# Kernel tuning notes

Measured on AMD Instinct MI355X. Metric: run time of the kernel, lower is better.

## Reference

```python
import jax, jax.numpy as jnp
import numpy as np
import math

D = 1024
FFN = 4096
NHEADS = 8
HEAD_DIM = D // NHEADS
RL_DIM = 4
LN_EPS = 1e-5


def _layer_norm(x, gamma, beta):
    mu = jnp.mean(x, axis=-1, keepdims=True)
    var = jnp.var(x, axis=-1, keepdims=True)
    return (x - mu) * jax.lax.rsqrt(var + LN_EPS) * gamma + beta


def setup_inputs() -> dict:
    key = jax.random.key(0)
    ks = jax.random.split(key, 12)
    B, L = 2, 2048
    s = 1.0 / math.sqrt(D)
    inp = {
        "h": jax.random.normal(ks[0], (B, L, D), dtype=jnp.float32),
        "rh": jax.random.normal(ks[1], (B, L, RL_DIM), dtype=jnp.float32),
        "Wq": jax.random.normal(ks[2], (D, D), dtype=jnp.float32) * s,
        "Wk": jax.random.normal(ks[3], (D, D), dtype=jnp.float32) * s,
        "Wv": jax.random.normal(ks[4], (D, D), dtype=jnp.float32) * s,
        "Wo": jax.random.normal(ks[5], (D, D), dtype=jnp.float32) * s,
        "Wrk": jax.random.normal(ks[6], (RL_DIM, RL_DIM), dtype=jnp.float32) * 0.5,
        "Wrq": jax.random.normal(ks[7], (RL_DIM, RL_DIM), dtype=jnp.float32) * 0.5,
        "W1": jax.random.normal(ks[8], (D, FFN), dtype=jnp.float32) * s,
        "b1": jnp.zeros((FFN,), dtype=jnp.float32),
        "W2": jax.random.normal(ks[9], (FFN, D), dtype=jnp.float32) / math.sqrt(FFN),
        "b2": jnp.zeros((D,), dtype=jnp.float32),
        "g1": jnp.ones((D,), dtype=jnp.float32),
        "be1": jnp.zeros((D,), dtype=jnp.float32),
        "g2": jnp.ones((D,), dtype=jnp.float32),
        "be2": jnp.zeros((D,), dtype=jnp.float32),
    }
    return inp


def reference(h, rh, Wq, Wk, Wv, Wo, Wrk, Wrq, W1, b1, W2, b2, g1, be1, g2, be2):
    B, L, _ = h.shape
    q = h @ Wq  # [B, L, D]
    k = h @ Wk
    v = h @ Wv
    # Faithful to the torch code: .view() reshapes (NOT transposes).
    q_ = q.reshape(B, NHEADS, L, HEAD_DIM)
    k_ = k.reshape(B, NHEADS, L, HEAD_DIM)
    v_ = v.reshape(B, NHEADS, L, HEAD_DIM)
    k_t = k_.reshape(B, NHEADS, HEAD_DIM, L)  # reshape, not transpose, as in source
    score = jnp.einsum("bnld,bndm->bnlm", q_, k_t) / math.sqrt(HEAD_DIM)
    # relative-position bias (rl=True path)
    r_k = rh @ Wrk  # [B, L, rl_dim]
    r_q = rh @ Wrq
    r_q_ = r_q[:, None]  # [B, 1, L, rl_dim]
    r_k_t = r_k[:, None].reshape(B, 1, RL_DIM, L)  # reshape, as in source
    score = score + jnp.einsum("bnlr,bnrm->bnlm", r_q_, r_k_t) / 2.0
    attn = jax.nn.softmax(score, axis=-1)
    context = jnp.einsum("bnlm,bnmd->bnld", attn, v_)
    h_sa = context.reshape(B, L, D) @ Wo
    h1 = _layer_norm(h_sa + h, g1, be1)
    hf = jax.nn.relu(h1 @ W1 + b1) @ W2 + b2
    h2 = _layer_norm(h1 + hf, g2, be2)
    return h2
```

## Files before the change

### kernel.cpp

```cpp
#include <hip/hip_runtime.h>

typedef __bf16 bf16;
typedef __bf16 bf16x8 __attribute__((ext_vector_type(8)));
typedef __bf16 bf16x4 __attribute__((ext_vector_type(4)));
typedef float  f32x4  __attribute__((ext_vector_type(4)));

#define D_     1024
#define FFN_   4096
#define NH_    8
#define HD_    128
#define L_     2048
#define B_     2
#define ROWS_  4096
#define PAIRS_ 16
#define KT_    64
#define PSTR   72
#define ALPHA_  0.08838834764831845f
#define RSCALE_ 5.656854249492381f

__device__ __forceinline__ void async16(const bf16* g, bf16* l) {
    __builtin_amdgcn_global_load_lds(
        (const __attribute__((address_space(1))) unsigned int*)g,
        (__attribute__((address_space(3))) unsigned int*)l, 16, 0, 0);
}
__device__ __forceinline__ f32x4 MFMA(bf16x8 a, bf16x8 b, f32x4 c) {
    return __builtin_amdgcn_mfma_f32_16x16x32_bf16(a, b, c, 0, 0, 0);
}

__global__ void cvt_bf16_kernel(const float* __restrict__ in, bf16* __restrict__ out) {
    long i = ((long)blockIdx.x * 256 + threadIdx.x) * 4;
    float4 v = *(const float4*)(in + i);
    bf16x4 o = {(bf16)v.x, (bf16)v.y, (bf16)v.z, (bf16)v.w};
    *(bf16x4*)(out + i) = o;
}

template<typename TI>
__global__ void transpose_to_bf16(const TI* __restrict__ in, bf16* __restrict__ out,
                                  int r, int c, long sIn, long sOut) {
    __shared__ bf16 t[32][33];
    long zi = (long)blockIdx.z * sIn;
    long zo = (long)blockIdx.z * sOut;
    int x0 = blockIdx.x * 32, y0 = blockIdx.y * 32;
    int tx = threadIdx.x & 31, ty = threadIdx.x >> 5;
#pragma unroll
    for (int i = 0; i < 4; i++)
        t[ty + i * 8][tx] = (bf16)in[zi + (long)(y0 + ty + i * 8) * c + x0 + tx];
    __syncthreads();
#pragma unroll
    for (int i = 0; i < 4; i++)
        out[zo + (long)(x0 + ty + i * 8) * r + y0 + tx] = t[tx][ty + i * 8];
}

__global__ void rqk_kernel(const float* __restrict__ rh, const float* __restrict__ Wrq,
                           const float* __restrict__ Wrk, float* __restrict__ rq,
                           float* __restrict__ rk) {
    int t = blockIdx.x * 256 + threadIdx.x;
    float4 r = *(const float4*)(rh + (long)t * 4);
    float q[4], k[4];
#pragma unroll
    for (int c = 0; c < 4; c++) {
        q[c] = r.x * Wrq[c] + r.y * Wrq[4 + c] + r.z * Wrq[8 + c] + r.w * Wrq[12 + c];
        k[c] = r.x * Wrk[c] + r.y * Wrk[4 + c] + r.z * Wrk[8 + c] + r.w * Wrk[12 + c];
    }
    float4 qo = {q[0], q[1], q[2], q[3]};
    float4 ko = {k[0], k[1], k[2], k[3]};
    *(float4*)(rq + (long)t * 4) = qo;
    *(float4*)(rk + (long)t * 4) = ko;
}

template<int BM, int EPI>
__launch_bounds__(256)
__global__ void gemm128(const bf16* __restrict__ A, const bf16* __restrict__ Bt,
                        void* __restrict__ Cv, const float* __restrict__ bias,
                        int M, int N, int K, int lda, int ldb,
                        long sA, long sB, long sC, float alpha) {
    constexpr int RF = (BM == 128) ? 4 : 2;
    __shared__ __align__(16) bf16 As[BM * 32];
    __shared__ __align__(16) bf16 Bs[128 * 32];
    const int tid  = threadIdx.x;
    const int wave = tid >> 6, lane = tid & 63;
    const int quad = lane >> 4, mr = lane & 15;
    const int bM = blockIdx.x * BM, bN = blockIdx.y * 128;
    A  += (long)blockIdx.z * sA;
    Bt += (long)blockIdx.z * sB;
    const int wr = (wave >> 1) * (BM / 2), wc = (wave & 1) * 64;

    f32x4 acc[RF][4];
#pragma unroll
    for (int r = 0; r < RF; r++)
#pragma unroll
        for (int c = 0; c < 4; c++) { f32x4 z = {0.f, 0.f, 0.f, 0.f}; acc[r][c] = z; }

    const int scol = (lane & 3) * 8;
    const bf16* Ag0; const bf16* Ag1 = nullptr;
    if (BM == 128) {
        const int srow = wave * 32 + (lane >> 2);
        Ag0 = A + (long)(bM + srow) * lda + scol;
        Ag1 = Ag0 + (long)16 * lda;
    } else {
        const int srow = wave * 16 + (lane >> 2);
        Ag0 = A + (long)(bM + srow) * lda + scol;
    }
    const int srowB = wave * 32 + (lane >> 2);
    const bf16* Bg0 = Bt + (long)(bN + srowB) * ldb + scol;
    const bf16* Bg1 = Bg0 + (long)16 * ldb;
    bf16* AsW = As + wave * (BM == 128 ? 1024 : 512);
    bf16* BsW = Bs + wave * 1024;

    for (int k0 = 0; k0 < K; k0 += 32) {
        if (BM == 128) { async16(Ag0, AsW); async16(Ag1, AsW + 512); Ag0 += 32; Ag1 += 32; }
        else           { async16(Ag0, AsW); Ag0 += 32; }
        async16(Bg0, BsW); async16(Bg1, BsW + 512);
        Bg0 += 32; Bg1 += 32;
        __syncthreads();
        bf16x8 af[RF], bfv[4];
#pragma unroll
        for (int r = 0; r < RF; r++)
            af[r] = *(const bf16x8*)(&As[(wr + r * 16 + mr) * 32 + quad * 8]);
#pragma unroll
        for (int c = 0; c < 4; c++)
            bfv[c] = *(const bf16x8*)(&Bs[(wc + c * 16 + mr) * 32 + quad * 8]);
#pragma unroll
        for (int r = 0; r < RF; r++)
#pragma unroll
            for (int c = 0; c < 4; c++)
                acc[r][c] = MFMA(af[r], bfv[c], acc[r][c]);
        __syncthreads();
    }

    const long zC = (long)blockIdx.z * sC;
    float bias_c[4];
    if (EPI & 1) {
#pragma unroll
        for (int c = 0; c < 4; c++) bias_c[c] = bias[bN + wc + c * 16 + mr];
    }
#pragma unroll
    for (int r = 0; r < RF; r++) {
#pragma unroll
        for (int c = 0; c < 4; c++) {
            const long col = bN + wc + c * 16 + mr;
#pragma unroll
            for (int i = 0; i < 4; i++) {
                const long row = bM + wr + r * 16 + quad * 4 + i;
                float v = acc[r][c][i] * alpha;
                if (EPI & 1) v += bias_c[c];
                if (EPI & 2) v = fmaxf(v, 0.f);
                if (EPI & 4) ((bf16*)Cv)[zC + row * (long)N + col] = (bf16)v;
                else         ((float*)Cv)[zC + row * (long)N + col] = v;
            }
        }
    }
}

template<int EPI>
__launch_bounds__(512, 2)
__global__ void gemm256(const bf16* __restrict__ A, const bf16* __restrict__ Bt,
                        void* __restrict__ Cv, const float* __restrict__ bias,
                        int M, int N, int K, int lda, int ldb,
                        long sA, long sB, long sC, float alpha) {
    __shared__ __align__(16) bf16 LA[4][256 * 32];
    __shared__ __align__(16) bf16 LB[4][256 * 32];
    const int tid = threadIdx.x, wave = tid >> 6, lane = tid & 63;
    const int quad = lane >> 4, mr = lane & 15;
    const int wr = wave >> 2, wc = wave & 3;
    const int bM = blockIdx.x * 256, bN = blockIdx.y * 256;
    (void)M;
    A  += (long)blockIdx.z * sA;
    Bt += (long)blockIdx.z * sB;

    const int srow = tid >> 2;
    const int sg   = (((tid & 3) ^ ((tid >> 3) & 3))) * 8;
    const bf16* Ag = A  + (long)(bM + srow) * lda + sg;
    const bf16* Bg = Bt + (long)(bN + srow) * ldb + sg;

    auto stageA = [&](int slot, int kt) {
        const bf16* s = Ag + kt * 32;
        async16(s,                   &LA[slot][wave * 512]);
        async16(s + (long)128 * lda, &LA[slot][4096 + wave * 512]);
    };
    auto stageB = [&](int slot, int kt) {
        const bf16* s = Bg + kt * 32;
        async16(s,                   &LB[slot][wave * 512]);
        async16(s + (long)128 * ldb, &LB[slot][4096 + wave * 512]);
    };

    f32x4 acc[8][4];
#pragma unroll
    for (int f = 0; f < 8; f++)
#pragma unroll
        for (int n = 0; n < 4; n++) { f32x4 z = {0.f, 0.f, 0.f, 0.f}; acc[f][n] = z; }

    const int gsw = (quad ^ ((mr >> 1) & 3)) * 8;

    stageA(0, 0); stageB(0, 0);
    stageA(1, 1); stageB(1, 1);
    stageA(2, 2); stageB(2, 2);
    asm volatile("s_waitcnt vmcnt(8)" ::: "memory");
    __builtin_amdgcn_s_barrier();

    const int NT = K >> 5;
    for (int t = 0; t < NT; ++t) {
        const int slot = t & 3;
        const bf16* As = &LA[slot][0];
        const bf16* Bs = &LB[slot][0];

        bf16x8 a0[4], bb[4];
#pragma unroll
        for (int f = 0; f < 4; f++)
            a0[f] = *(const bf16x8*)(As + (wr * 128 + f * 16 + mr) * 32 + gsw);
#pragma unroll
        for (int n = 0; n < 4; n++)
            bb[n] = *(const bf16x8*)(Bs + (wc * 64 + n * 16 + mr) * 32 + gsw);
        if (t + 3 < NT) stageA((t + 3) & 3, t + 3);
        __builtin_amdgcn_s_barrier();
        asm volatile("s_waitcnt lgkmcnt(0)" ::: "memory");
        __builtin_amdgcn_sched_barrier(0);
        __builtin_amdgcn_s_setprio(1);
#pragma unroll
        for (int f = 0; f < 4; f++)
#pragma unroll
            for (int n = 0; n < 4; n++)
                acc[f][n] = MFMA(a0[f], bb[n], acc[f][n]);
        __builtin_amdgcn_s_setprio(0);
        __builtin_amdgcn_s_barrier();

        bf16x8 a1[4];
#pragma unroll
        for (int f = 0; f < 4; f++)
            a1[f] = *(const bf16x8*)(As + (wr * 128 + 64 + f * 16 + mr) * 32 + gsw);
        if (t + 3 < NT) stageB((t + 3) & 3, t + 3);
        __builtin_amdgcn_s_barrier();
        asm volatile("s_waitcnt lgkmcnt(0)" ::: "memory");
        __builtin_amdgcn_sched_barrier(0);
        __builtin_amdgcn_s_setprio(1);
#pragma unroll
        for (int f = 0; f < 4; f++)
#pragma unroll
            for (int n = 0; n < 4; n++)
                acc[4 + f][n] = MFMA(a1[f], bb[n], acc[4 + f][n]);
        __builtin_amdgcn_s_setprio(0);
        if (t < NT - 3)       asm volatile("s_waitcnt vmcnt(8)" ::: "memory");
        else if (t == NT - 3) asm volatile("s_waitcnt vmcnt(4)" ::: "memory");
        else if (t == NT - 2) asm volatile("s_waitcnt vmcnt(0)" ::: "memory");
        __builtin_amdgcn_s_barrier();
    }

    const long zC = (long)blockIdx.z * sC;
    float bias_c[4];
    if (EPI & 1) {
#pragma unroll
        for (int n = 0; n < 4; n++) bias_c[n] = bias[bN + wc * 64 + n * 16 + mr];
    }
#pragma unroll
    for (int f = 0; f < 8; f++) {
#pragma unroll
        for (int n = 0; n < 4; n++) {
            const long col = bN + wc * 64 + n * 16 + mr;
#pragma unroll
            for (int i = 0; i < 4; i++) {
                const long row = bM + wr * 128 + f * 16 + quad * 4 + i;
                float v = acc[f][n][i] * alpha;
                if (EPI & 1) v += bias_c[n];
                if (EPI & 2) v = fmaxf(v, 0.f);
                if (EPI & 4) ((bf16*)Cv)[zC + row * (long)N + col] = (bf16)v;
                else         ((float*)Cv)[zC + row * (long)N + col] = v;
            }
        }
    }
}

template<int SPLIT>
__launch_bounds__(256, 1)
__global__ void flash_attn(const bf16* __restrict__ qb, const bf16* __restrict__ kT,
                           const bf16* __restrict__ vT, const float* __restrict__ rq,
                           const float* __restrict__ rk, bf16* __restrict__ ctx,
                           float* __restrict__ opart, float* __restrict__ osum) {
    __shared__ __align__(16) bf16  Ksh[KT_ * HD_];
    __shared__ __align__(16) bf16  Vsh[HD_ * KT_];
    __shared__ __align__(16) float rks[4 * KT_];
    __shared__ __align__(16) bf16  Ps[4][32 * PSTR];

    const int tid = threadIdx.x, wave = tid >> 6, lane = tid & 63;
    const int quad = lane >> 4, mr = lane & 15;
    const int pair = blockIdx.y, b = pair >> 3;
    const int ksp = blockIdx.z;
    const int bQ = blockIdx.x * 128;
    const long PB = (long)pair * L_ * HD_;
    const bf16* Qg = qb + PB;
    const bf16* Kg = kT + PB;
    const bf16* Vg = vT + PB;
    const float* rkb = rk + (long)b * L_ * 4;

    bf16x8 Qf[2][4], Qe[2];
#pragma unroll
    for (int f = 0; f < 2; f++) {
#pragma unroll
        for (int t = 0; t < 4; t++)
            Qf[f][t] = *(const bf16x8*)(Qg + (long)(bQ + wave * 32 + f * 16 + mr) * HD_ + t * 32 + quad * 8);
        bf16x8 z = {};
        if (quad == 0) {
            float4 v = *(const float4*)(rq + ((long)b * L_ + bQ + wave * 32 + f * 16 + mr) * 4);
            z[0] = (bf16)(v.x * RSCALE_); z[1] = (bf16)(v.y * RSCALE_);
            z[2] = (bf16)(v.z * RSCALE_); z[3] = (bf16)(v.w * RSCALE_);
        }
        Qe[f] = z;
    }

    bf16x8 ones;
#pragma unroll
    for (int j = 0; j < 8; j++) ones[j] = (bf16)1.0f;

    f32x4 O[2][8], Os[2];
#pragma unroll
    for (int f = 0; f < 2; f++) {
#pragma unroll
        for (int c = 0; c < 8; c++) { f32x4 z = {0.f, 0.f, 0.f, 0.f}; O[f][c] = z; }
        f32x4 z = {0.f, 0.f, 0.f, 0.f}; Os[f] = z;
    }

    const int tile0 = ksp * ((L_ / KT_) / SPLIT);
    const int tile1 = tile0 + (L_ / KT_) / SPLIT;
    for (int kt = tile0; kt < tile1; kt++) {
        const int kt0 = kt * KT_;
#pragma unroll
        for (int it = 0; it < 4; it++) {
            int G = it * 256 + tid;
            int r1 = G >> 4, g1 = (G & 15) ^ (r1 & 15);
            async16(Kg + (long)(kt0 + r1) * HD_ + g1 * 8, &Ksh[(it * 256 + wave * 64) * 8]);
            int r2 = G >> 3, g2 = (G & 7) ^ (r2 & 7);
            async16(Vg + (long)r2 * L_ + kt0 + g2 * 8, &Vsh[(it * 256 + wave * 64) * 8]);
        }
        if (tid < 64) {
            int r3 = tid >> 4, g3 = tid & 15;
            async16((const bf16*)(rkb + (long)r3 * L_ + kt0 + g3 * 4), (bf16*)&rks[0]);
        }
        __syncthreads();

        bf16* PsW = Ps[wave];

        f32x4 sc[4][2];
#pragma unroll
        for (int c = 0; c < 4; c++) {
            f32x4 s0 = {0.f, 0.f, 0.f, 0.f}, s1 = s0;
#pragma unroll
            for (int t = 0; t < 4; t++) {
                bf16x8 kf = *(const bf16x8*)(Ksh + (c * 16 + mr) * HD_ + (((t * 4 + quad) ^ mr) * 8));
                s0 = MFMA(Qf[0][t], kf, s0);
                s1 = MFMA(Qf[1][t], kf, s1);
            }
            bf16x8 ke = {};
            if (quad == 0) {
                ke[0] = (bf16)rks[0 * KT_ + c * 16 + mr];
                ke[1] = (bf16)rks[1 * KT_ + c * 16 + mr];
                ke[2] = (bf16)rks[2 * KT_ + c * 16 + mr];
                ke[3] = (bf16)rks[3 * KT_ + c * 16 + mr];
            }
            s0 = MFMA(Qe[0], ke, s0);
            s1 = MFMA(Qe[1], ke, s1);
            sc[c][0] = s0; sc[c][1] = s1;
        }

#pragma unroll
        for (int f = 0; f < 2; f++) {
#pragma unroll
            for (int i = 0; i < 4; i++) {
                const int prow = (f * 16 + quad * 4 + i) * PSTR;
                PsW[prow + 0 * 16 + mr] = (bf16)__expf(sc[0][f][i] * ALPHA_);
                PsW[prow + 1 * 16 + mr] = (bf16)__expf(sc[1][f][i] * ALPHA_);
                PsW[prow + 2 * 16 + mr] = (bf16)__expf(sc[2][f][i] * ALPHA_);
                PsW[prow + 3 * 16 + mr] = (bf16)__expf(sc[3][f][i] * ALPHA_);
            }
        }

#pragma unroll
        for (int t = 0; t < 2; t++) {
            bf16x8 pf0 = *(const bf16x8*)(PsW + (0 * 16 + mr) * PSTR + t * 32 + quad * 8);
            bf16x8 pf1 = *(const bf16x8*)(PsW + (1 * 16 + mr) * PSTR + t * 32 + quad * 8);
            Os[0] = MFMA(pf0, ones, Os[0]);
            Os[1] = MFMA(pf1, ones, Os[1]);
#pragma unroll
            for (int c2 = 0; c2 < 8; c2++) {
                bf16x8 vf = *(const bf16x8*)(Vsh + (c2 * 16 + mr) * KT_ + (((t * 4 + quad) ^ (mr & 7)) * 8));
                O[0][c2] = MFMA(pf0, vf, O[0][c2]);
                O[1][c2] = MFMA(pf1, vf, O[1][c2]);
            }
        }
        __syncthreads();
    }

    if (SPLIT == 1) {
        bf16* Cg = ctx + PB;
#pragma unroll
        for (int f = 0; f < 2; f++)
#pragma unroll
            for (int i = 0; i < 4; i++) {
                const float inv = 1.f / Os[f][i];
                const long row = bQ + wave * 32 + f * 16 + quad * 4 + i;
#pragma unroll
                for (int c2 = 0; c2 < 8; c2++)
                    Cg[row * HD_ + c2 * 16 + mr] = (bf16)(O[f][c2][i] * inv);
            }
    } else {
        float* Og = opart + (long)ksp * ((long)PAIRS_ * L_ * HD_) + PB;
        float* Sg = osum + (long)ksp * (PAIRS_ * L_) + pair * L_;
#pragma unroll
        for (int f = 0; f < 2; f++)
#pragma unroll
            for (int i = 0; i < 4; i++) {
                const long row = bQ + wave * 32 + f * 16 + quad * 4 + i;
#pragma unroll
                for (int c2 = 0; c2 < 8; c2++)
                    Og[row * HD_ + c2 * 16 + mr] = O[f][c2][i];
                if (mr == 0) Sg[row] = Os[f][i];
            }
    }
}

__global__ void flash_reduce(const float* __restrict__ op, const float* __restrict__ os,
                             bf16* __restrict__ ctx) {
    const long PLHD = (long)PAIRS_ * L_ * HD_;
    long e = ((long)blockIdx.x * 256 + threadIdx.x) * 4;
    long row = e >> 7;
    float4 a = *(const float4*)(op + e);
    float4 b = *(const float4*)(op + PLHD + e);
    float inv = 1.f / (os[row] + os[(long)PAIRS_ * L_ + row]);
    bf16x4 o = {(bf16)((a.x + b.x) * inv), (bf16)((a.y + b.y) * inv),
                (bf16)((a.z + b.z) * inv), (bf16)((a.w + b.w) * inv)};
    *(bf16x4*)(ctx + e) = o;
}

__global__ void layernorm_res(const float* __restrict__ x1, const float* __restrict__ x2,
                              const float* __restrict__ g, const float* __restrict__ be,
                              float* __restrict__ outf, bf16* __restrict__ outb) {
    const int row = blockIdx.x, tid = threadIdx.x;
    const long base = (long)row * D_ + tid * 4;
    float4 a = *(const float4*)(x1 + base);
    float4 b = *(const float4*)(x2 + base);
    float x[4] = {a.x + b.x, a.y + b.y, a.z + b.z, a.w + b.w};
    float s = x[0] + x[1] + x[2] + x[3];
    float s2 = x[0] * x[0] + x[1] * x[1] + x[2] * x[2] + x[3] * x[3];
#pragma unroll
    for (int off = 32; off; off >>= 1) { s += __shfl_xor(s, off, 64); s2 += __shfl_xor(s2, off, 64); }
    __shared__ float ps[4], ps2[4];
    int wave = tid >> 6, lane = tid & 63;
    if (lane == 0) { ps[wave] = s; ps2[wave] = s2; }
    __syncthreads();
    s  = ps[0] + ps[1] + ps[2] + ps[3];
    s2 = ps2[0] + ps2[1] + ps2[2] + ps2[3];
    float mean = s * (1.f / D_);
    float var  = s2 * (1.f / D_) - mean * mean;
    float rstd = rsqrtf(var + 1e-5f);
    float4 gg = *(const float4*)(g + tid * 4);
    float4 bb = *(const float4*)(be + tid * 4);
    float y0 = (x[0] - mean) * rstd * gg.x + bb.x;
    float y1 = (x[1] - mean) * rstd * gg.y + bb.y;
    float y2 = (x[2] - mean) * rstd * gg.z + bb.z;
    float y3 = (x[3] - mean) * rstd * gg.w + bb.w;
    float4 yo = {y0, y1, y2, y3};
    *(float4*)(outf + base) = yo;
    bf16x4 ob = {(bf16)y0, (bf16)y1, (bf16)y2, (bf16)y3};
    *(bf16x4*)(outb + base) = ob;
}

template<int SK>
__global__ void layernorm_res2(const float* __restrict__ parts, const float* __restrict__ b2,
                               const float* __restrict__ x2, const float* __restrict__ g,
                               const float* __restrict__ be, float* __restrict__ outf) {
    const int row = blockIdx.x, tid = threadIdx.x;
    const long base = (long)row * D_ + tid * 4;
    float4 a = *(const float4*)(parts + base);
#pragma unroll
    for (int z = 1; z < SK; z++) {
        float4 p = *(const float4*)(parts + (long)z * ROWS_ * D_ + base);
        a.x += p.x; a.y += p.y; a.z += p.z; a.w += p.w;
    }
    float4 bb2 = *(const float4*)(b2 + tid * 4);
    float4 b = *(const float4*)(x2 + base);
    float x[4] = {a.x + bb2.x + b.x, a.y + bb2.y + b.y, a.z + bb2.z + b.z, a.w + bb2.w + b.w};
    float s = x[0] + x[1] + x[2] + x[3];
    float s2 = x[0] * x[0] + x[1] * x[1] + x[2] * x[2] + x[3] * x[3];
#pragma unroll
    for (int off = 32; off; off >>= 1) { s += __shfl_xor(s, off, 64); s2 += __shfl_xor(s2, off, 64); }
    __shared__ float ps[4], ps2[4];
    int wave = tid >> 6, lane = tid & 63;
    if (lane == 0) { ps[wave] = s; ps2[wave] = s2; }
    __syncthreads();
    s  = ps[0] + ps[1] + ps[2] + ps[3];
    s2 = ps2[0] + ps2[1] + ps2[2] + ps2[3];
    float mean = s * (1.f / D_);
    float var  = s2 * (1.f / D_) - mean * mean;
    float rstd = rsqrtf(var + 1e-5f);
    float4 gg = *(const float4*)(g + tid * 4);
    float4 bb = *(const float4*)(be + tid * 4);
    float4 yo = {(x[0] - mean) * rstd * gg.x + bb.x, (x[1] - mean) * rstd * gg.y + bb.y,
                 (x[2] - mean) * rstd * gg.z + bb.z, (x[3] - mean) * rstd * gg.w + bb.w};
    *(float4*)(outf + base) = yo;
}

extern "C" void kernel_launch(void* const* d_in, const int* in_sizes, int n_in,
                              void* d_out, int out_size, void* d_ws, size_t ws_size,
                              hipStream_t stream) {
    (void)in_sizes; (void)n_in; (void)out_size;
    const float* h   = (const float*)d_in[0];
    const float* rh  = (const float*)d_in[1];
    const float* Wq  = (const float*)d_in[2];
    const float* Wk  = (const float*)d_in[3];
    const float* Wv  = (const float*)d_in[4];
    const float* Wo  = (const float*)d_in[5];
    const float* Wrk = (const float*)d_in[6];
    const float* Wrq = (const float*)d_in[7];
    const float* W1  = (const float*)d_in[8];
    const float* b1  = (const float*)d_in[9];
    const float* W2  = (const float*)d_in[10];
    const float* b2  = (const float*)d_in[11];
    const float* g1  = (const float*)d_in[12];
    const float* be1 = (const float*)d_in[13];
    const float* g2  = (const float*)d_in[14];
    const float* be2 = (const float*)d_in[15];

    char* w = (char*)d_ws;
    size_t used = 0;
    auto alloc = [&](size_t bytes) { char* p = w + used; used += (bytes + 255) & ~(size_t)255; return p; };
    bf16*  hb   = (bf16*)alloc((size_t)ROWS_ * D_ * 2);
    bf16*  Wqt  = (bf16*)alloc((size_t)D_ * D_ * 2);
    bf16*  Wkt  = (bf16*)alloc((size_t)D_ * D_ * 2);
    bf16*  Wvt  = (bf16*)alloc((size_t)D_ * D_ * 2);
    bf16*  Wot  = (bf16*)alloc((size_t)D_ * D_ * 2);
    bf16*  W1t  = (bf16*)alloc((size_t)D_ * FFN_ * 2);
    bf16*  W2t  = (bf16*)alloc((size_t)FFN_ * D_ * 2);
    bf16*  qb   = (bf16*)alloc((size_t)ROWS_ * D_ * 2);
    bf16*  kb   = (bf16*)alloc((size_t)ROWS_ * D_ * 2);
    bf16*  vb   = (bf16*)alloc((size_t)ROWS_ * D_ * 2);
    bf16*  kT   = (bf16*)alloc((size_t)ROWS_ * D_ * 2);
    bf16*  vT   = (bf16*)alloc((size_t)ROWS_ * D_ * 2);
    float* rq   = (float*)alloc((size_t)ROWS_ * 4 * 4);
    float* rk   = (float*)alloc((size_t)ROWS_ * 4 * 4);
    float* h1   = (float*)alloc((size_t)ROWS_ * D_ * 4);

    const size_t psz    = (size_t)ROWS_ * D_ * 4;
    const size_t PLHD   = (size_t)PAIRS_ * L_ * HD_;
    const size_t needKS = 2 * PLHD * 4 + 2 * (size_t)PAIRS_ * L_ * 4;
    const size_t avail  = (ws_size > used) ? ws_size - used : 0;
    const int SK = (avail >= 4 * psz) ? 4 : (avail >= 2 * psz) ? 2 : 1;
    size_t region = (size_t)SK * psz;
    const int KS = (avail >= (needKS > region ? needKS : region)) ? 2 : 1;
    if (KS == 2 && needKS > region) region = needKS;
    float* P = (float*)alloc(region);
    float* hsa   = P;
    float* Opart = P;
    float* Osum  = P + 2 * PLHD;
    bf16* ctx = hb;
    bf16* mid = qb;
    bf16* h1b = hb;

    const dim3 blk(256);
    const dim3 blk512(512);
    const long BH = (long)L_ * HD_;

    cvt_bf16_kernel<<<ROWS_ * D_ / 1024, blk, 0, stream>>>(h, hb);
    transpose_to_bf16<float><<<dim3(32, 32, 1), blk, 0, stream>>>(Wq, Wqt, D_, D_, 0, 0);
    transpose_to_bf16<float><<<dim3(32, 32, 1), blk, 0, stream>>>(Wk, Wkt, D_, D_, 0, 0);
    transpose_to_bf16<float><<<dim3(32, 32, 1), blk, 0, stream>>>(Wv, Wvt, D_, D_, 0, 0);
    transpose_to_bf16<float><<<dim3(32, 32, 1), blk, 0, stream>>>(Wo, Wot, D_, D_, 0, 0);
    transpose_to_bf16<float><<<dim3(128, 32, 1), blk, 0, stream>>>(W1, W1t, D_, FFN_, 0, 0);
    transpose_to_bf16<float><<<dim3(32, 128, 1), blk, 0, stream>>>(W2, W2t, FFN_, D_, 0, 0);
    rqk_kernel<<<ROWS_ / 256, blk, 0, stream>>>(rh, Wrq, Wrk, rq, rk);
    gemm256<4><<<dim3(16, 4, 3), blk512, 0, stream>>>(hb, Wqt, qb, nullptr,
        ROWS_, D_, D_, D_, D_, 0, (long)D_ * D_, (long)ROWS_ * D_, 1.f);
    transpose_to_bf16<bf16><<<dim3(64, 4, PAIRS_), blk, 0, stream>>>(kb, kT, HD_, L_, BH, BH);
    transpose_to_bf16<bf16><<<dim3(4, 64, PAIRS_), blk, 0, stream>>>(vb, vT, L_, HD_, BH, BH);
    if (KS == 2) {
        flash_attn<2><<<dim3(16, 16, 2), blk, 0, stream>>>(qb, kT, vT, rq, rk, ctx, Opart, Osum);
        flash_reduce<<<PAIRS_ * L_ * HD_ / 1024, blk, 0, stream>>>(Opart, Osum, ctx);
    } else {
        flash_attn<1><<<dim3(16, 16, 1), blk, 0, stream>>>(qb, kT, vT, rq, rk, ctx, Opart, Osum);
    }
    gemm128<64, 0><<<dim3(64, 8, 1), blk, 0, stream>>>(ctx, Wot, hsa, nullptr,
        ROWS_, D_, D_, D_, D_, 0, 0, 0, 1.f);
    layernorm_res<<<ROWS_, blk, 0, stream>>>(hsa, h, g1, be1, h1, h1b);
    gemm256<7><<<dim3(16, 16, 1), blk512, 0, stream>>>(h1b, W1t, mid, b1,
        ROWS_, FFN_, D_, D_, D_, 0, 0, 0, 1.f);
    {
        const int KC = FFN_ / SK;
        if (SK == 4) {
            gemm256<0><<<dim3(16, 4, 4), blk512, 0, stream>>>(mid, W2t, P, nullptr,
                ROWS_, D_, KC, FFN_, FFN_, KC, KC, (long)ROWS_ * D_, 1.f);
            layernorm_res2<4><<<ROWS_, blk, 0, stream>>>(P, b2, h1, g2, be2, (float*)d_out);
        } else if (SK == 2) {
            gemm256<0><<<dim3(16, 4, 2), blk512, 0, stream>>>(mid, W2t, P, nullptr,
                ROWS_, D_, KC, FFN_, FFN_, KC, KC, (long)ROWS_ * D_, 1.f);
            layernorm_res2<2><<<ROWS_, blk, 0, stream>>>(P, b2, h1, g2, be2, (float*)d_out);
        } else {
            gemm128<128, 0><<<dim3(32, 8, 1), blk, 0, stream>>>(mid, W2t, P, nullptr,
                ROWS_, D_, FFN_, FFN_, FFN_, 0, 0, 0, 1.f);
            layernorm_res2<1><<<ROWS_, blk, 0, stream>>>(P, b2, h1, g2, be2, (float*)d_out);
        }
    }
}
```

Before: 382.4 us.

## Double-buffer K tiles and overlap V loads with QK compute in flash attention

Flash attention now keeps two shared-memory buffers for the K tile and the rk bias. The next tile's K and rk are prefetched while the current tile's scores are computed, and the V load is issued before the QK MFMAs so it can land during them. The single end-of-iteration __syncthreads is replaced by explicit vmcnt waits and barriers, and s_setprio raises wave priority around the MFMA blocks. This hides global-to-LDS latency at the cost of extra LDS use and more delicate hand-counted waits.

```diff
diff --git a/kernel.cpp b/kernel.cpp
--- a/kernel.cpp
+++ b/kernel.cpp
@@ -275,9 +275,9 @@
                            const bf16* __restrict__ vT, const float* __restrict__ rq,
                            const float* __restrict__ rk, bf16* __restrict__ ctx,
                            float* __restrict__ opart, float* __restrict__ osum) {
-    __shared__ __align__(16) bf16  Ksh[KT_ * HD_];
+    __shared__ __align__(16) bf16  Ksh[2][KT_ * HD_];
     __shared__ __align__(16) bf16  Vsh[HD_ * KT_];
-    __shared__ __align__(16) float rks[4 * KT_];
+    __shared__ __align__(16) float rks[2][4 * KT_];
     __shared__ __align__(16) bf16  Ps[4][32 * PSTR];
 
     const int tid = threadIdx.x, wave = tid >> 6, lane = tid & 63;
@@ -320,45 +320,75 @@
 
     const int tile0 = ksp * ((L_ / KT_) / SPLIT);
     const int tile1 = tile0 + (L_ / KT_) / SPLIT;
-    for (int kt = tile0; kt < tile1; kt++) {
-        const int kt0 = kt * KT_;
+
+    {
+        const int kt0 = tile0 * KT_;
 #pragma unroll
         for (int it = 0; it < 4; it++) {
             int G = it * 256 + tid;
             int r1 = G >> 4, g1 = (G & 15) ^ (r1 & 15);
-            async16(Kg + (long)(kt0 + r1) * HD_ + g1 * 8, &Ksh[(it * 256 + wave * 64) * 8]);
+            async16(Kg + (long)(kt0 + r1) * HD_ + g1 * 8, &Ksh[0][(it * 256 + wave * 64) * 8]);
+        }
+        if (tid < 64) {
+            int r3 = tid >> 4, g3 = tid & 15;
+            async16((const bf16*)(rkb + (long)r3 * L_ + kt0 + g3 * 4), (bf16*)&rks[0][0]);
+        }
+        asm volatile("s_waitcnt vmcnt(0)" ::: "memory");
+        __builtin_amdgcn_s_barrier();
+    }
+
+    for (int kt = tile0; kt < tile1; kt++) {
+        const int cur = kt & 1, nxt = cur ^ 1;
+        const int kt0 = kt * KT_;
+        const bool hn = (kt + 1 < tile1);
+
+#pragma unroll
+        for (int it = 0; it < 4; it++) {
+            int G = it * 256 + tid;
             int r2 = G >> 3, g2 = (G & 7) ^ (r2 & 7);
             async16(Vg + (long)r2 * L_ + kt0 + g2 * 8, &Vsh[(it * 256 + wave * 64) * 8]);
         }
-        if (tid < 64) {
-            int r3 = tid >> 4, g3 = tid & 15;
-            async16((const bf16*)(rkb + (long)r3 * L_ + kt0 + g3 * 4), (bf16*)&rks[0]);
-        }
-        __syncthreads();
+        if (hn) {
+            const int kn0 = kt0 + KT_;
+#pragma unroll
+            for (int it = 0; it < 4; it++) {
+                int G = it * 256 + tid;
+                int r1 = G >> 4, g1 = (G & 15) ^ (r1 & 15);
+                async16(Kg + (long)(kn0 + r1) * HD_ + g1 * 8, &Ksh[nxt][(it * 256 + wave * 64) * 8]);
+            }
+            if (tid < 64) {
+                int r3 = tid >> 4, g3 = tid & 15;
+                async16((const bf16*)(rkb + (long)r3 * L_ + kn0 + g3 * 4), (bf16*)&rks[nxt][0]);
+            }
+        }
 
         bf16* PsW = Ps[wave];
+        const bf16*  Kcur = Ksh[cur];
+        const float* rkc  = rks[cur];
 
         f32x4 sc[4][2];
+        __builtin_amdgcn_s_setprio(1);
 #pragma unroll
         for (int c = 0; c < 4; c++) {
             f32x4 s0 = {0.f, 0.f, 0.f, 0.f}, s1 = s0;
 #pragma unroll
             for (int t = 0; t < 4; t++) {
-                bf16x8 kf = *(const bf16x8*)(Ksh + (c * 16 + mr) * HD_ + (((t * 4 + quad) ^ mr) * 8));
+                bf16x8 kf = *(const bf16x8*)(Kcur + (c * 16 + mr) * HD_ + (((t * 4 + quad) ^ mr) * 8));
                 s0 = MFMA(Qf[0][t], kf, s0);
                 s1 = MFMA(Qf[1][t], kf, s1);
             }
             bf16x8 ke = {};
             if (quad == 0) {
-                ke[0] = (bf16)rks[0 * KT_ + c * 16 + mr];
-                ke[1] = (bf16)rks[1 * KT_ + c * 16 + mr];
-                ke[2] = (bf16)rks[2 * KT_ + c * 16 + mr];
-                ke[3] = (bf16)rks[3 * KT_ + c * 16 + mr];
+                ke[0] = (bf16)rkc[0 * KT_ + c * 16 + mr];
+                ke[1] = (bf16)rkc[1 * KT_ + c * 16 + mr];
+                ke[2] = (bf16)rkc[2 * KT_ + c * 16 + mr];
+                ke[3] = (bf16)rkc[3 * KT_ + c * 16 + mr];
             }
             s0 = MFMA(Qe[0], ke, s0);
             s1 = MFMA(Qe[1], ke, s1);
             sc[c][0] = s0; sc[c][1] = s1;
         }
+        __builtin_amdgcn_s_setprio(0);
 
 #pragma unroll
         for (int f = 0; f < 2; f++) {
@@ -372,6 +402,11 @@
             }
         }
 
+        if (hn) asm volatile("s_waitcnt vmcnt(4)" ::: "memory");
+        else    asm volatile("s_waitcnt vmcnt(0)" ::: "memory");
+        __builtin_amdgcn_s_barrier();
+
+        __builtin_amdgcn_s_setprio(1);
 #pragma unroll
         for (int t = 0; t < 2; t++) {
             bf16x8 pf0 = *(const bf16x8*)(PsW + (0 * 16 + mr) * PSTR + t * 32 + quad * 8);
@@ -385,7 +420,12 @@
                 O[1][c2] = MFMA(pf1, vf, O[1][c2]);
             }
         }
-        __syncthreads();
+        __builtin_amdgcn_s_setprio(0);
+
+        if (hn) {
+            asm volatile("s_waitcnt vmcnt(0)" ::: "memory");
+            __builtin_amdgcn_s_barrier();
+        }
     }
 
     if (SPLIT == 1) {
```

Result: slower. 408.9 us (+6.9%).

## Add 512-thread flash attention with 4-way KV split and generic reduce

Applied to the files above, without the earlier changes.

Adds a flash attention variant whose blocks have 8 waves covering 256 query rows, so each K/V tile loaded into LDS is reused by twice as many query rows. The kernel splits the key range four ways and writes partial outputs and sums that a templated reduce kernel combines. The partial buffers need more workspace, and the host picks the 4-way split only when enough is available. The reduce kernel and the partial buffers now carry four fp32 copies of the context, which adds memory traffic. The grid keeps the same block count (8x16x4), but each block is larger.

```diff
diff --git a/kernel.cpp b/kernel.cpp
--- a/kernel.cpp
+++ b/kernel.cpp
@@ -270,6 +270,139 @@
 }
 
 template<int SPLIT>
+__launch_bounds__(512, 1)
+__global__ void flash_attn256(const bf16* __restrict__ qb, const bf16* __restrict__ kT,
+                              const bf16* __restrict__ vT, const float* __restrict__ rq,
+                              const float* __restrict__ rk,
+                              float* __restrict__ opart, float* __restrict__ osum) {
+    __shared__ __align__(16) bf16  Ksh[KT_ * HD_];
+    __shared__ __align__(16) bf16  Vsh[HD_ * KT_];
+    __shared__ __align__(16) float rks[4 * KT_];
+    __shared__ __align__(16) bf16  Ps[8][32 * PSTR];
+
+    const int tid = threadIdx.x, wave = tid >> 6, lane = tid & 63;
+    const int quad = lane >> 4, mr = lane & 15;
+    const int pair = blockIdx.y, b = pair >> 3;
+    const int ksp = blockIdx.z;
+    const int bQ = blockIdx.x * 256;
+    const long PB = (long)pair * L_ * HD_;
+    const bf16* Qg = qb + PB;
+    const bf16* Kg = kT + PB;
+    const bf16* Vg = vT + PB;
+    const float* rkb = rk + (long)b * L_ * 4;
+
+    bf16x8 Qf[2][4], Qe[2];
+#pragma unroll
+    for (int f = 0; f < 2; f++) {
+#pragma unroll
+        for (int t = 0; t < 4; t++)
+            Qf[f][t] = *(const bf16x8*)(Qg + (long)(bQ + wave * 32 + f * 16 + mr) * HD_ + t * 32 + quad * 8);
+        bf16x8 z = {};
+        if (quad == 0) {
+            float4 v = *(const float4*)(rq + ((long)b * L_ + bQ + wave * 32 + f * 16 + mr) * 4);
+            z[0] = (bf16)(v.x * RSCALE_); z[1] = (bf16)(v.y * RSCALE_);
+            z[2] = (bf16)(v.z * RSCALE_); z[3] = (bf16)(v.w * RSCALE_);
+        }
+        Qe[f] = z;
+    }
+
+    bf16x8 ones;
+#pragma unroll
+    for (int j = 0; j < 8; j++) ones[j] = (bf16)1.0f;
+
+    f32x4 O[2][8], Os[2];
+#pragma unroll
+    for (int f = 0; f < 2; f++) {
+#pragma unroll
+        for (int c = 0; c < 8; c++) { f32x4 z = {0.f, 0.f, 0.f, 0.f}; O[f][c] = z; }
+        f32x4 z = {0.f, 0.f, 0.f, 0.f}; Os[f] = z;
+    }
+
+    const int tile0 = ksp * ((L_ / KT_) / SPLIT);
+    const int tile1 = tile0 + (L_ / KT_) / SPLIT;
+    for (int kt = tile0; kt < tile1; kt++) {
+        const int kt0 = kt * KT_;
+#pragma unroll
+        for (int it = 0; it < 2; it++) {
+            int G = it * 512 + tid;
+            int r1 = G >> 4, g1 = (G & 15) ^ (r1 & 15);
+            async16(Kg + (long)(kt0 + r1) * HD_ + g1 * 8, &Ksh[(it * 512 + wave * 64) * 8]);
+            int r2 = G >> 3, g2 = (G & 7) ^ (r2 & 7);
+            async16(Vg + (long)r2 * L_ + kt0 + g2 * 8, &Vsh[(it * 512 + wave * 64) * 8]);
+        }
+        if (tid < 64) {
+            int r3 = tid >> 4, g3 = tid & 15;
+            async16((const bf16*)(rkb + (long)r3 * L_ + kt0 + g3 * 4), (bf16*)&rks[0]);
+        }
+        __syncthreads();
+
+        bf16* PsW = Ps[wave];
+
+        f32x4 sc[4][2];
+#pragma unroll
+        for (int c = 0; c < 4; c++) {
+            f32x4 s0 = {0.f, 0.f, 0.f, 0.f}, s1 = s0;
+#pragma unroll
+            for (int t = 0; t < 4; t++) {
+                bf16x8 kf = *(const bf16x8*)(Ksh + (c * 16 + mr) * HD_ + (((t * 4 + quad) ^ mr) * 8));
+                s0 = MFMA(Qf[0][t], kf, s0);
+                s1 = MFMA(Qf[1][t], kf, s1);
+            }
+            bf16x8 ke = {};
+            if (quad == 0) {
+                ke[0] = (bf16)rks[0 * KT_ + c * 16 + mr];
+                ke[1] = (bf16)rks[1 * KT_ + c * 16 + mr];
+                ke[2] = (bf16)rks[2 * KT_ + c * 16 + mr];
+                ke[3] = (bf16)rks[3 * KT_ + c * 16 + mr];
+            }
+            s0 = MFMA(Qe[0], ke, s0);
+            s1 = MFMA(Qe[1], ke, s1);
+            sc[c][0] = s0; sc[c][1] = s1;
+        }
+
+#pragma unroll
+        for (int f = 0; f < 2; f++) {
+#pragma unroll
+            for (int i = 0; i < 4; i++) {
+                const int prow = (f * 16 + quad * 4 + i) * PSTR;
+                PsW[prow + 0 * 16 + mr] = (bf16)__expf(sc[0][f][i] * ALPHA_);
+                PsW[prow + 1 * 16 + mr] = (bf16)__expf(sc[1][f][i] * ALPHA_);
+                PsW[prow + 2 * 16 + mr] = (bf16)__expf(sc[2][f][i] * ALPHA_);
+                PsW[prow + 3 * 16 + mr] = (bf16)__expf(sc[3][f][i] * ALPHA_);
+            }
+        }
+
+#pragma unroll
+        for (int t = 0; t < 2; t++) {
+            bf16x8 pf0 = *(const bf16x8*)(PsW + (0 * 16 + mr) * PSTR + t * 32 + quad * 8);
+            bf16x8 pf1 = *(const bf16x8*)(PsW + (1 * 16 + mr) * PSTR + t * 32 + quad * 8);
+            Os[0] = MFMA(pf0, ones, Os[0]);
+            Os[1] = MFMA(pf1, ones, Os[1]);
+#pragma unroll
+            for (int c2 = 0; c2 < 8; c2++) {
+                bf16x8 vf = *(const bf16x8*)(Vsh + (c2 * 16 + mr) * KT_ + (((t * 4 + quad) ^ (mr & 7)) * 8));
+                O[0][c2] = MFMA(pf0, vf, O[0][c2]);
+                O[1][c2] = MFMA(pf1, vf, O[1][c2]);
+            }
+        }
+        __syncthreads();
+    }
+
+    float* Og = opart + (long)ksp * ((long)PAIRS_ * L_ * HD_) + PB;
+    float* Sg = osum + (long)ksp * (PAIRS_ * L_) + pair * L_;
+#pragma unroll
+    for (int f = 0; f < 2; f++)
+#pragma unroll
+        for (int i = 0; i < 4; i++) {
+            const long row = bQ + wave * 32 + f * 16 + quad * 4 + i;
+#pragma unroll
+            for (int c2 = 0; c2 < 8; c2++)
+                Og[row * HD_ + c2 * 16 + mr] = O[f][c2][i];
+            if (mr == 0) Sg[row] = Os[f][i];
+        }
+}
+
+template<int SPLIT>
 __launch_bounds__(256, 1)
 __global__ void flash_attn(const bf16* __restrict__ qb, const bf16* __restrict__ kT,
                            const bf16* __restrict__ vT, const float* __restrict__ rq,
@@ -416,16 +549,23 @@
     }
 }
 
+template<int KS>
 __global__ void flash_reduce(const float* __restrict__ op, const float* __restrict__ os,
                              bf16* __restrict__ ctx) {
     const long PLHD = (long)PAIRS_ * L_ * HD_;
     long e = ((long)blockIdx.x * 256 + threadIdx.x) * 4;
     long row = e >> 7;
     float4 a = *(const float4*)(op + e);
-    float4 b = *(const float4*)(op + PLHD + e);
-    float inv = 1.f / (os[row] + os[(long)PAIRS_ * L_ + row]);
-    bf16x4 o = {(bf16)((a.x + b.x) * inv), (bf16)((a.y + b.y) * inv),
-                (bf16)((a.z + b.z) * inv), (bf16)((a.w + b.w) * inv)};
+    float s = os[row];
+#pragma unroll
+    for (int z = 1; z < KS; z++) {
+        float4 p = *(const float4*)(op + (long)z * PLHD + e);
+        a.x += p.x; a.y += p.y; a.z += p.z; a.w += p.w;
+        s += os[(long)z * PAIRS_ * L_ + row];
+    }
+    float inv = 1.f / s;
+    bf16x4 o = {(bf16)(a.x * inv), (bf16)(a.y * inv),
+                (bf16)(a.z * inv), (bf16)(a.w * inv)};
     *(bf16x4*)(ctx + e) = o;
 }
 
@@ -537,18 +677,25 @@
     float* rk   = (float*)alloc((size_t)ROWS_ * 4 * 4);
     float* h1   = (float*)alloc((size_t)ROWS_ * D_ * 4);
 
-    const size_t psz    = (size_t)ROWS_ * D_ * 4;
-    const size_t PLHD   = (size_t)PAIRS_ * L_ * HD_;
-    const size_t needKS = 2 * PLHD * 4 + 2 * (size_t)PAIRS_ * L_ * 4;
-    const size_t avail  = (ws_size > used) ? ws_size - used : 0;
+    const size_t psz     = (size_t)ROWS_ * D_ * 4;
+    const size_t PLHD    = (size_t)PAIRS_ * L_ * HD_;
+    const size_t needKS4 = 4 * PLHD * 4 + 4 * (size_t)PAIRS_ * L_ * 4;
+    const size_t needKS2 = 2 * PLHD * 4 + 2 * (size_t)PAIRS_ * L_ * 4;
+    const size_t avail   = (ws_size > used) ? ws_size - used : 0;
     const int SK = (avail >= 4 * psz) ? 4 : (avail >= 2 * psz) ? 2 : 1;
     size_t region = (size_t)SK * psz;
-    const int KS = (avail >= (needKS > region ? needKS : region)) ? 2 : 1;
-    if (KS == 2 && needKS > region) region = needKS;
+    int KS;
+    if (avail >= (needKS4 > region ? needKS4 : region)) {
+        KS = 4; if (needKS4 > region) region = needKS4;
+    } else if (avail >= (needKS2 > region ? needKS2 : region)) {
+        KS = 2; if (needKS2 > region) region = needKS2;
+    } else {
+        KS = 1;
+    }
     float* P = (float*)alloc(region);
     float* hsa   = P;
     float* Opart = P;
-    float* Osum  = P + 2 * PLHD;
+    float* Osum  = P + (size_t)KS * PLHD;
     bf16* ctx = hb;
     bf16* mid = qb;
     bf16* h1b = hb;
@@ -569,9 +716,12 @@
         ROWS_, D_, D_, D_, D_, 0, (long)D_ * D_, (long)ROWS_ * D_, 1.f);
     transpose_to_bf16<bf16><<<dim3(64, 4, PAIRS_), blk, 0, stream>>>(kb, kT, HD_, L_, BH, BH);
     transpose_to_bf16<bf16><<<dim3(4, 64, PAIRS_), blk, 0, stream>>>(vb, vT, L_, HD_, BH, BH);
-    if (KS == 2) {
+    if (KS == 4) {
+        flash_attn256<4><<<dim3(8, 16, 4), blk512, 0, stream>>>(qb, kT, vT, rq, rk, Opart, Osum);
+        flash_reduce<4><<<PAIRS_ * L_ * HD_ / 1024, blk, 0, stream>>>(Opart, Osum, ctx);
+    } else if (KS == 2) {
         flash_attn<2><<<dim3(16, 16, 2), blk, 0, stream>>>(qb, kT, vT, rq, rk, ctx, Opart, Osum);
-        flash_reduce<<<PAIRS_ * L_ * HD_ / 1024, blk, 0, stream>>>(Opart, Osum, ctx);
+        flash_reduce<2><<<PAIRS_ * L_ * HD_ / 1024, blk, 0, stream>>>(Opart, Osum, ctx);
     } else {
         flash_attn<1><<<dim3(16, 16, 1), blk, 0, stream>>>(qb, kT, vT, rq, rk, ctx, Opart, Osum);
     }
```

After: 392.6 us. 2.7% more time.
